# Optimization experiments

Measured on AMD Instinct MI355X. Metric: run time of the kernel, lower is better.

Reference implementation:

```python
import jax, jax.numpy as jnp
import numpy as np

IMAGE_SIZE = 320
SIGMA = 0.01      # soft-edge width in NDC units (~1.6 px at 320 res)
CHUNK = 128       # faces per scan step (bounds peak memory)


def setup_inputs() -> dict:
    key = jax.random.key(0)
    k1, k2 = jax.random.split(key)
    verts = jax.random.normal(k1, (4, 778, 3), dtype=jnp.float32) * 0.5
    faces = jax.random.randint(k2, (1538, 3), 0, 778, dtype=jnp.int32)
    return {"verts": verts, "faces": faces}


def _silhouette(verts, faces):
    B = verts.shape[0]
    S = IMAGE_SIZE
    # NMR.forward flips the y axis of verts before rendering
    v = verts * jnp.array([1.0, -1.0, 1.0], dtype=verts.dtype)
    xy = v[..., :2]  # orthographic projection (perspective=False)
    F = faces.shape[0]
    n_chunks = -(-F // CHUNK)
    Fp = n_chunks * CHUNK
    faces_p = jnp.pad(faces, ((0, Fp - F), (0, 0)))
    valid = (jnp.arange(Fp) < F).astype(verts.dtype)
    tri = xy[:, faces_p]  # [B, Fp, 3, 2]
    tri = jnp.moveaxis(tri.reshape(B, n_chunks, CHUNK, 3, 2), 1, 0)  # [nc,B,C,3,2]
    valid = valid.reshape(n_chunks, CHUNK)
    # pixel centers in NDC [-1, 1]
    lin = (jnp.arange(S, dtype=verts.dtype) + 0.5) / S * 2.0 - 1.0
    py, px = jnp.meshgrid(lin, lin, indexing="ij")
    px = px.reshape(-1)  # [P]
    py = py.reshape(-1)

    def edge_d(a, b, sgn):
        # signed distance of every pixel to oriented edge a->b: [B, C, P]
        ex = b[..., 0] - a[..., 0]
        ey = b[..., 1] - a[..., 1]
        inv_len = 1.0 / (jnp.sqrt(ex * ex + ey * ey) + 1e-8)
        d = (ex[..., None] * (py[None, None, :] - a[..., 1:2])
             - ey[..., None] * (px[None, None, :] - a[..., 0:1]))
        return sgn[..., None] * d * inv_len[..., None]

    def body(acc, chunk):
        tri_c, m = chunk  # [B,C,3,2], [C]
        v0, v1, v2 = tri_c[..., 0, :], tri_c[..., 1, :], tri_c[..., 2, :]
        # orientation sign so CW / CCW triangles are handled uniformly
        area2 = ((v1[..., 0] - v0[..., 0]) * (v2[..., 1] - v0[..., 1])
                 - (v1[..., 1] - v0[..., 1]) * (v2[..., 0] - v0[..., 0]))
        sgn = jnp.sign(area2)
        logp = (jax.nn.log_sigmoid(edge_d(v0, v1, sgn) / SIGMA)
                + jax.nn.log_sigmoid(edge_d(v1, v2, sgn) / SIGMA)
                + jax.nn.log_sigmoid(edge_d(v2, v0, sgn) / SIGMA))
        prob = jnp.clip(jnp.exp(logp) * m[None, :, None], 0.0, 1.0 - 1e-6)
        return acc + jnp.sum(jnp.log1p(-prob), axis=1), None

    acc0 = jnp.zeros((B, S * S), dtype=verts.dtype)
    acc, _ = jax.lax.scan(body, acc0, (tri, valid))
    # silhouette = 1 - prod_f (1 - coverage_f), accumulated in log space
    return (1.0 - jnp.exp(acc)).reshape(B, S, S)


def reference(verts, faces):
    return _silhouette(verts, faces)
```

## Files before the change

### kernel.cpp

```cpp
#include <hip/hip_runtime.h>
#include <math.h>


#define IMG_S 320
#define N_FACES 1538
#define N_VERTS 778
#define N_BATCH 4
#define FP 1600
#define TILE 8
#define CHUNK_F 384
#define N_CHUNKS 4
#define MAXB 388
#define NWAVE 4
#define INV_SIGMA 100.0f
#define T_CUT 12.0f
#define ACC_CUT_P 2.2603294e-6f
#define LOG2_1EM6 -19.9315686f

__global__ __launch_bounds__(256)
void prep_faces(const float* __restrict__ verts,
                const int* __restrict__ faces,
                float4* __restrict__ gE0,
                float4* __restrict__ gE1,
                float4* __restrict__ gE2)
{
    const int f = blockIdx.x * 256 + threadIdx.x;
    const int b = blockIdx.z;
    if (f >= N_FACES) return;

    const float* vb = verts + (size_t)b * N_VERTS * 3;
    const int i0 = faces[f * 3 + 0];
    const int i1 = faces[f * 3 + 1];
    const int i2 = faces[f * 3 + 2];
    const float x0 = vb[i0 * 3 + 0], y0 = -vb[i0 * 3 + 1];
    const float x1 = vb[i1 * 3 + 0], y1 = -vb[i1 * 3 + 1];
    const float x2 = vb[i2 * 3 + 0], y2 = -vb[i2 * 3 + 1];

    const float dx1 = x1 - x0, dy1 = y1 - y0;
    const float dx2 = x2 - x0, dy2 = y2 - y0;
    const float area2 = __builtin_fmaf(dx1, dy2, -__fmul_rn(dy1, dx2));
    const float sgn = (area2 > 0.0f) ? 1.0f : ((area2 < 0.0f) ? -1.0f : 0.0f);

    const size_t o = (size_t)b * FP + f;
    {
        const float ex = x1 - x0, ey = y1 - y0;
        const float s = sgn * INV_SIGMA / (sqrtf(ex * ex + ey * ey) + 1e-8f);
        gE0[o] = make_float4(-s * ey, s * ex, s * (ey * x0 - ex * y0), 0.0f);
    }
    {
        const float ex = x2 - x1, ey = y2 - y1;
        const float s = sgn * INV_SIGMA / (sqrtf(ex * ex + ey * ey) + 1e-8f);
        gE1[o] = make_float4(-s * ey, s * ex, s * (ey * x1 - ex * y1), 0.0f);
    }
    {
        const float ex = x0 - x2, ey = y0 - y2;
        const float s = sgn * INV_SIGMA / (sqrtf(ex * ex + ey * ey) + 1e-8f);
        gE2[o] = make_float4(-s * ey, s * ex, s * (ey * x2 - ex * y2), 0.0f);
    }
}

__global__ __launch_bounds__(256)
void silhouette_ws(const float4* __restrict__ gE0,
                   const float4* __restrict__ gE1,
                   const float4* __restrict__ gE2,
                   float* __restrict__ out)
{
    __shared__ float4 sE0[MAXB];
    __shared__ float4 sE1[MAXB];
    __shared__ float4 sE2[MAXB];
    __shared__ float sAcc[256];
    __shared__ int sCount;
    __shared__ int sAlive;
    __shared__ int sCover;

    const int t    = threadIdx.x;
    const int wave = t >> 6;
    const int lane = t & 63;
    const int p    = t & 63;
    const int plx  = p & 7;
    const int ply  = p >> 3;
    const int b    = blockIdx.z;
    const int gx   = blockIdx.x * TILE + plx;
    const int gy   = blockIdx.y * TILE + ply;

    const float w  = 2.0f / IMG_S;
    const float px = (gx + 0.5f) * w - 1.0f;
    const float py = (gy + 0.5f) * w - 1.0f;
    const float cx = (blockIdx.x * TILE + 4) * w - 1.0f;
    const float cy = (blockIdx.y * TILE + 4) * w - 1.0f;
    const float rr = 3.5f * w;

    const float4* gb0 = gE0 + (size_t)b * FP;
    const float4* gb1 = gE1 + (size_t)b * FP;
    const float4* gb2 = gE2 + (size_t)b * FP;

    float acc = 1.0f;

    for (int c = 0; c < N_CHUNKS; ++c) {
        const int base = c * CHUNK_F;
        const int end  = (c == N_CHUNKS - 1) ? N_FACES : base + CHUNK_F;

        sAcc[t] = acc;
        if (t == 0) { sCount = 0; sAlive = 0; sCover = 0; }
        __syncthreads();

        const float tot = sAcc[p] * sAcc[p + 64] * sAcc[p + 128] * sAcc[p + 192];
        const bool alive = (tot > ACC_CUT_P);
        if (alive) sAlive = 1;
        __syncthreads();

        if (sAlive == 0) break;

        for (int fb = base; fb < end; fb += 256) {
            const int fc = fb + t;
            const bool vald = (fc < end);
            const int fcc = vald ? fc : (end - 1);
            const float4 e0 = gb0[fcc];
            const float4 e1 = gb1[fcc];
            const float4 e2 = gb2[fcc];
            const float c0 = fmaf(e0.x, cx, fmaf(e0.y, cy, e0.z));
            const float c1 = fmaf(e1.x, cx, fmaf(e1.y, cy, e1.z));
            const float c2 = fmaf(e2.x, cx, fmaf(e2.y, cy, e2.z));
            const float r0 = rr * (fabsf(e0.x) + fabsf(e0.y));
            const float r1 = rr * (fabsf(e1.x) + fabsf(e1.y));
            const float r2 = rr * (fabsf(e2.x) + fabsf(e2.y));
            const float m_hi = fminf(c0 + r0, fminf(c1 + r1, c2 + r2));
            const float m_lo = fminf(c0 - r0, fminf(c1 - r1, c2 - r2));
            const bool isCov  = vald && (m_lo > T_CUT);
            const bool isBand = vald && !isCov && (m_hi > -T_CUT);

            const unsigned long long mb = __ballot(isBand);
            int wbase = 0;
            if (lane == 0) {
                const int nw = __popcll(mb);
                if (nw) wbase = atomicAdd(&sCount, nw);
            }
            wbase = __shfl(wbase, 0);
            if (isBand) {
                const int pos = wbase + __popcll(mb & ((1ull << lane) - 1ull));
                sE0[pos] = e0;
                sE1[pos] = e1;
                sE2[pos] = e2;
            }
            const unsigned long long mc = __ballot(isCov);
            if (lane == 0) {
                const int ncv = __popcll(mc);
                if (ncv) atomicAdd(&sCover, ncv);
            }
        }
        __syncthreads();

        const float coverF = exp2f((float)sCover * LOG2_1EM6);
        bool live = alive && (acc * coverF > ACC_CUT_P);
        if (wave == 0) acc *= coverF;

        const int n = sCount;
        int j = wave;
        while (j < n) {
            if (__ballot(live) == 0ull) break;
            const int j1 = j + NWAVE;
            const int j1c = (j1 < n) ? j1 : j;
            const float4 A0 = sE0[j],   A1 = sE1[j],   A2 = sE2[j];
            const float4 B0 = sE0[j1c], B1 = sE1[j1c], B2 = sE2[j1c];
            {
                const float xa = fmaf(A0.x, px, fmaf(A0.y, py, A0.z));
                const float xb = fmaf(A1.x, px, fmaf(A1.y, py, A1.z));
                const float xc = fmaf(A2.x, px, fmaf(A2.y, py, A2.z));
                const float m = fminf(xa, fminf(xb, xc));
                if (live && m > -T_CUT) {
                    const float da = 1.0f + __expf(-xa);
                    const float db = 1.0f + __expf(-xb);
                    const float dc = 1.0f + __expf(-xc);
                    const float f = fmaxf(
                        1.0f - __builtin_amdgcn_rcpf(da * db * dc), 1e-6f);
                    acc *= f;
                    live = (acc > ACC_CUT_P);
                }
            }
            if (j1 < n) {
                const float xa = fmaf(B0.x, px, fmaf(B0.y, py, B0.z));
                const float xb = fmaf(B1.x, px, fmaf(B1.y, py, B1.z));
                const float xc = fmaf(B2.x, px, fmaf(B2.y, py, B2.z));
                const float m = fminf(xa, fminf(xb, xc));
                if (live && m > -T_CUT) {
                    const float da = 1.0f + __expf(-xa);
                    const float db = 1.0f + __expf(-xb);
                    const float dc = 1.0f + __expf(-xc);
                    const float f = fmaxf(
                        1.0f - __builtin_amdgcn_rcpf(da * db * dc), 1e-6f);
                    acc *= f;
                    live = (acc > ACC_CUT_P);
                }
            }
            j += 2 * NWAVE;
        }
    }

    sAcc[t] = acc;
    __syncthreads();
    if (t < 64) {
        const float tot = sAcc[p] * sAcc[p + 64] * sAcc[p + 128] * sAcc[p + 192];
        out[(size_t)b * (IMG_S * IMG_S) + (size_t)gy * IMG_S + gx] = 1.0f - tot;
    }
}

extern "C" void kernel_launch(void* const* d_in, const int* in_sizes, int n_in,
                              void* d_out, int out_size, void* d_ws, size_t ws_size,
                              hipStream_t stream) {
    const float* verts = (const float*)d_in[0];
    const int* faces = (const int*)d_in[1];
    float* out = (float*)d_out;

    float4* gE0 = (float4*)d_ws;
    float4* gE1 = gE0 + (size_t)N_BATCH * FP;
    float4* gE2 = gE1 + (size_t)N_BATCH * FP;

    dim3 pgrid((N_FACES + 255) / 256, 1, N_BATCH);
    prep_faces<<<pgrid, 256, 0, stream>>>(verts, faces, gE0, gE1, gE2);

    dim3 grid(IMG_S / TILE, IMG_S / TILE, N_BATCH);
    silhouette_ws<<<grid, 256, 0, stream>>>(gE0, gE1, gE2, out);
}
```

Baseline: 81.74 us.

## Classify active edges per tile and specialize per-face sigmoid evaluation

Edge coefficients are pre-scaled by log2(e)/sigma so the inner loop uses exp2 directly. During binning, each band face records which of its edges can still affect the tile (the others are treated as saturated at 1), and the per-pixel loop branches uniformly on that count to evaluate one, two or three sigmoids. Per-pixel live tracking is replaced by a wave-wide early-exit check on the accumulator. This cuts exp, rcp and LDS reads for faces near a single edge, at the cost of extra branching and a slightly different approximation near the cutoffs.

```diff
diff --git a/kernel.cpp b/kernel.cpp
--- a/kernel.cpp
+++ b/kernel.cpp
@@ -12,8 +12,9 @@
 #define N_CHUNKS 4
 #define MAXB 388
 #define NWAVE 4
-#define INV_SIGMA 100.0f
-#define T_CUT 12.0f
+#define SCALE_S 144.2695041f
+#define T_CUT_S 17.31234049f
+#define T_ACT_S 18.75503553f
 #define ACC_CUT_P 2.2603294e-6f
 #define LOG2_1EM6 -19.9315686f
 
@@ -44,17 +45,17 @@
     const size_t o = (size_t)b * FP + f;
     {
         const float ex = x1 - x0, ey = y1 - y0;
-        const float s = sgn * INV_SIGMA / (sqrtf(ex * ex + ey * ey) + 1e-8f);
+        const float s = sgn * SCALE_S / (sqrtf(ex * ex + ey * ey) + 1e-8f);
         gE0[o] = make_float4(-s * ey, s * ex, s * (ey * x0 - ex * y0), 0.0f);
     }
     {
         const float ex = x2 - x1, ey = y2 - y1;
-        const float s = sgn * INV_SIGMA / (sqrtf(ex * ex + ey * ey) + 1e-8f);
+        const float s = sgn * SCALE_S / (sqrtf(ex * ex + ey * ey) + 1e-8f);
         gE1[o] = make_float4(-s * ey, s * ex, s * (ey * x1 - ex * y1), 0.0f);
     }
     {
         const float ex = x0 - x2, ey = y0 - y2;
-        const float s = sgn * INV_SIGMA / (sqrtf(ex * ex + ey * ey) + 1e-8f);
+        const float s = sgn * SCALE_S / (sqrtf(ex * ex + ey * ey) + 1e-8f);
         gE2[o] = make_float4(-s * ey, s * ex, s * (ey * x2 - ex * y2), 0.0f);
     }
 }
@@ -126,8 +127,8 @@
             const float r2 = rr * (fabsf(e2.x) + fabsf(e2.y));
             const float m_hi = fminf(c0 + r0, fminf(c1 + r1, c2 + r2));
             const float m_lo = fminf(c0 - r0, fminf(c1 - r1, c2 - r2));
-            const bool isCov  = vald && (m_lo > T_CUT);
-            const bool isBand = vald && !isCov && (m_hi > -T_CUT);
+            const bool isCov  = vald && (m_lo > T_CUT_S);
+            const bool isBand = vald && !isCov && (m_hi > -T_CUT_S);
 
             const unsigned long long mb = __ballot(isBand);
             int wbase = 0;
@@ -138,8 +139,15 @@
             wbase = __shfl(wbase, 0);
             if (isBand) {
                 const int pos = wbase + __popcll(mb & ((1ull << lane) - 1ull));
-                sE0[pos] = e0;
-                sE1[pos] = e1;
+                const bool a0 = (c0 - r0) <= T_ACT_S;
+                const bool a1 = (c1 - r1) <= T_ACT_S;
+                const bool a2 = (c2 - r2) <= T_ACT_S;
+                const int cnt = (int)a0 + (int)a1 + (int)a2;
+                float4 first  = a0 ? e0 : (a1 ? e1 : e2);
+                const float4 second = a0 ? (a1 ? e1 : e2) : e2;
+                first.w = __int_as_float(cnt);
+                sE0[pos] = first;
+                sE1[pos] = second;
                 sE2[pos] = e2;
             }
             const unsigned long long mc = __ballot(isCov);
@@ -151,45 +159,74 @@
         __syncthreads();
 
         const float coverF = exp2f((float)sCover * LOG2_1EM6);
-        bool live = alive && (acc * coverF > ACC_CUT_P);
         if (wave == 0) acc *= coverF;
 
         const int n = sCount;
         int j = wave;
         while (j < n) {
-            if (__ballot(live) == 0ull) break;
+            if (__ballot(acc > ACC_CUT_P) == 0ull) break;
             const int j1 = j + NWAVE;
             const int j1c = (j1 < n) ? j1 : j;
-            const float4 A0 = sE0[j],   A1 = sE1[j],   A2 = sE2[j];
-            const float4 B0 = sE0[j1c], B1 = sE1[j1c], B2 = sE2[j1c];
+            const float4 A0 = sE0[j];
+            const float4 B0 = sE0[j1c];
             {
-                const float xa = fmaf(A0.x, px, fmaf(A0.y, py, A0.z));
-                const float xb = fmaf(A1.x, px, fmaf(A1.y, py, A1.z));
-                const float xc = fmaf(A2.x, px, fmaf(A2.y, py, A2.z));
-                const float m = fminf(xa, fminf(xb, xc));
-                if (live && m > -T_CUT) {
-                    const float da = 1.0f + __expf(-xa);
-                    const float db = 1.0f + __expf(-xb);
-                    const float dc = 1.0f + __expf(-xc);
-                    const float f = fmaxf(
-                        1.0f - __builtin_amdgcn_rcpf(da * db * dc), 1e-6f);
-                    acc *= f;
-                    live = (acc > ACC_CUT_P);
+                const float x0 = fmaf(A0.x, px, fmaf(A0.y, py, A0.z));
+                const int cnt = __builtin_amdgcn_readfirstlane(
+                                    __float_as_int(A0.w));
+                if (cnt == 1) {
+                    acc *= fmaxf(__builtin_amdgcn_rcpf(1.0f + exp2f(x0)),
+                                 1e-6f);
+                } else {
+                    const float4 A1 = sE1[j];
+                    const float x1 = fmaf(A1.x, px, fmaf(A1.y, py, A1.z));
+                    if (cnt == 2) {
+                        const float d0 = 1.0f + exp2f(-x0);
+                        const float d1 = 1.0f + exp2f(-x1);
+                        acc *= fmaxf(
+                            1.0f - __builtin_amdgcn_rcpf(d0 * d1), 1e-6f);
+                    } else {
+                        const float4 A2 = sE2[j];
+                        const float x2 = fmaf(A2.x, px, fmaf(A2.y, py, A2.z));
+                        const float m = fminf(x0, fminf(x1, x2));
+                        if (m > -T_CUT_S) {
+                            const float d0 = 1.0f + exp2f(-x0);
+                            const float d1 = 1.0f + exp2f(-x1);
+                            const float d2 = 1.0f + exp2f(-x2);
+                            acc *= fmaxf(
+                                1.0f - __builtin_amdgcn_rcpf(d0 * d1 * d2),
+                                1e-6f);
+                        }
+                    }
                 }
             }
             if (j1 < n) {
-                const float xa = fmaf(B0.x, px, fmaf(B0.y, py, B0.z));
-                const float xb = fmaf(B1.x, px, fmaf(B1.y, py, B1.z));
-                const float xc = fmaf(B2.x, px, fmaf(B2.y, py, B2.z));
-                const float m = fminf(xa, fminf(xb, xc));
-                if (live && m > -T_CUT) {
-                    const float da = 1.0f + __expf(-xa);
-                    const float db = 1.0f + __expf(-xb);
-                    const float dc = 1.0f + __expf(-xc);
-                    const float f = fmaxf(
-                        1.0f - __builtin_amdgcn_rcpf(da * db * dc), 1e-6f);
-                    acc *= f;
-                    live = (acc > ACC_CUT_P);
+                const float x0 = fmaf(B0.x, px, fmaf(B0.y, py, B0.z));
+                const int cnt = __builtin_amdgcn_readfirstlane(
+                                    __float_as_int(B0.w));
+                if (cnt == 1) {
+                    acc *= fmaxf(__builtin_amdgcn_rcpf(1.0f + exp2f(x0)),
+                                 1e-6f);
+                } else {
+                    const float4 B1 = sE1[j1c];
+                    const float x1 = fmaf(B1.x, px, fmaf(B1.y, py, B1.z));
+                    if (cnt == 2) {
+                        const float d0 = 1.0f + exp2f(-x0);
+                        const float d1 = 1.0f + exp2f(-x1);
+                        acc *= fmaxf(
+                            1.0f - __builtin_amdgcn_rcpf(d0 * d1), 1e-6f);
+                    } else {
+                        const float4 B2 = sE2[j1c];
+                        const float x2 = fmaf(B2.x, px, fmaf(B2.y, py, B2.z));
+                        const float m = fminf(x0, fminf(x1, x2));
+                        if (m > -T_CUT_S) {
+                            const float d0 = 1.0f + exp2f(-x0);
+                            const float d1 = 1.0f + exp2f(-x1);
+                            const float d2 = 1.0f + exp2f(-x2);
+                            acc *= fmaxf(
+                                1.0f - __builtin_amdgcn_rcpf(d0 * d1 * d2),
+                                1e-6f);
+                        }
+                    }
                 }
             }
             j += 2 * NWAVE;
```

New measurement: 134.1 us. 64.1% more time.

## Split band faces into single-edge and multi-edge lists with base-2 edge scaling

Applied to the files above, without the earlier changes.

Edge coefficients are pre-scaled by log2(e)/sigma so the per-pixel sigmoid uses exp2 directly. During face binning, each band face is classified by how many of its edges can be active over the tile. Faces where at most one edge matters store only that edge and are evaluated with a single exp and rcp per pixel. Faces with two or more active edges go into a second list packed from the top of a shared buffer. The per-pixel live flag is replaced by a wave-level ballot on acc, which removes per-face branching but lets pixels that have already saturated keep multiplying.

```diff
diff --git a/kernel.cpp b/kernel.cpp
--- a/kernel.cpp
+++ b/kernel.cpp
@@ -12,8 +12,9 @@
 #define N_CHUNKS 4
 #define MAXB 388
 #define NWAVE 4
-#define INV_SIGMA 100.0f
-#define T_CUT 12.0f
+#define SCALE_S 144.2695041f
+#define T_CUT_S 17.31234049f
+#define T_ACT_S 18.75503553f
 #define ACC_CUT_P 2.2603294e-6f
 #define LOG2_1EM6 -19.9315686f
 
@@ -44,17 +45,17 @@
     const size_t o = (size_t)b * FP + f;
     {
         const float ex = x1 - x0, ey = y1 - y0;
-        const float s = sgn * INV_SIGMA / (sqrtf(ex * ex + ey * ey) + 1e-8f);
+        const float s = sgn * SCALE_S / (sqrtf(ex * ex + ey * ey) + 1e-8f);
         gE0[o] = make_float4(-s * ey, s * ex, s * (ey * x0 - ex * y0), 0.0f);
     }
     {
         const float ex = x2 - x1, ey = y2 - y1;
-        const float s = sgn * INV_SIGMA / (sqrtf(ex * ex + ey * ey) + 1e-8f);
+        const float s = sgn * SCALE_S / (sqrtf(ex * ex + ey * ey) + 1e-8f);
         gE1[o] = make_float4(-s * ey, s * ex, s * (ey * x1 - ex * y1), 0.0f);
     }
     {
         const float ex = x0 - x2, ey = y0 - y2;
-        const float s = sgn * INV_SIGMA / (sqrtf(ex * ex + ey * ey) + 1e-8f);
+        const float s = sgn * SCALE_S / (sqrtf(ex * ex + ey * ey) + 1e-8f);
         gE2[o] = make_float4(-s * ey, s * ex, s * (ey * x2 - ex * y2), 0.0f);
     }
 }
@@ -65,11 +66,10 @@
                    const float4* __restrict__ gE2,
                    float* __restrict__ out)
 {
-    __shared__ float4 sE0[MAXB];
-    __shared__ float4 sE1[MAXB];
-    __shared__ float4 sE2[MAXB];
+    __shared__ float4 sBuf[3 * MAXB];
     __shared__ float sAcc[256];
-    __shared__ int sCount;
+    __shared__ int sCount1;
+    __shared__ int sCount3;
     __shared__ int sAlive;
     __shared__ int sCover;
 
@@ -101,7 +101,7 @@
         const int end  = (c == N_CHUNKS - 1) ? N_FACES : base + CHUNK_F;
 
         sAcc[t] = acc;
-        if (t == 0) { sCount = 0; sAlive = 0; sCover = 0; }
+        if (t == 0) { sCount1 = 0; sCount3 = 0; sAlive = 0; sCover = 0; }
         __syncthreads();
 
         const float tot = sAcc[p] * sAcc[p + 64] * sAcc[p + 128] * sAcc[p + 192];
@@ -126,21 +126,44 @@
             const float r2 = rr * (fabsf(e2.x) + fabsf(e2.y));
             const float m_hi = fminf(c0 + r0, fminf(c1 + r1, c2 + r2));
             const float m_lo = fminf(c0 - r0, fminf(c1 - r1, c2 - r2));
-            const bool isCov  = vald && (m_lo > T_CUT);
-            const bool isBand = vald && !isCov && (m_hi > -T_CUT);
-
-            const unsigned long long mb = __ballot(isBand);
-            int wbase = 0;
-            if (lane == 0) {
-                const int nw = __popcll(mb);
-                if (nw) wbase = atomicAdd(&sCount, nw);
-            }
-            wbase = __shfl(wbase, 0);
-            if (isBand) {
-                const int pos = wbase + __popcll(mb & ((1ull << lane) - 1ull));
-                sE0[pos] = e0;
-                sE1[pos] = e1;
-                sE2[pos] = e2;
+            const bool isCov  = vald && (m_lo > T_CUT_S);
+            const bool isBand = vald && !isCov && (m_hi > -T_CUT_S);
+
+            const bool a0 = (c0 - r0) <= T_ACT_S;
+            const bool a1 = (c1 - r1) <= T_ACT_S;
+            const bool a2 = (c2 - r2) <= T_ACT_S;
+            const int cnt = (int)a0 + (int)a1 + (int)a2;
+            const bool isS = isBand && (cnt <= 1);
+            const bool isT = isBand && (cnt >= 2);
+
+            {
+                const unsigned long long ms = __ballot(isS);
+                int wb = 0;
+                if (lane == 0) {
+                    const int nw = __popcll(ms);
+                    if (nw) wb = atomicAdd(&sCount1, nw);
+                }
+                wb = __shfl(wb, 0);
+                if (isS) {
+                    const int pos = wb + __popcll(ms & ((1ull << lane) - 1ull));
+                    sBuf[pos] = a0 ? e0 : (a1 ? e1 : e2);
+                }
+            }
+            {
+                const unsigned long long mt = __ballot(isT);
+                int wb = 0;
+                if (lane == 0) {
+                    const int nw = __popcll(mt);
+                    if (nw) wb = atomicAdd(&sCount3, nw);
+                }
+                wb = __shfl(wb, 0);
+                if (isT) {
+                    const int pos = wb + __popcll(mt & ((1ull << lane) - 1ull));
+                    const int bix = 3 * MAXB - 3 * (pos + 1);
+                    sBuf[bix + 0] = e0;
+                    sBuf[bix + 1] = e1;
+                    sBuf[bix + 2] = e2;
+                }
             }
             const unsigned long long mc = __ballot(isCov);
             if (lane == 0) {
@@ -151,45 +174,61 @@
         __syncthreads();
 
         const float coverF = exp2f((float)sCover * LOG2_1EM6);
-        bool live = alive && (acc * coverF > ACC_CUT_P);
         if (wave == 0) acc *= coverF;
 
-        const int n = sCount;
+        const int n1 = sCount1;
         int j = wave;
-        while (j < n) {
-            if (__ballot(live) == 0ull) break;
+        while (j < n1) {
+            if (__ballot(acc > ACC_CUT_P) == 0ull) break;
             const int j1 = j + NWAVE;
-            const int j1c = (j1 < n) ? j1 : j;
-            const float4 A0 = sE0[j],   A1 = sE1[j],   A2 = sE2[j];
-            const float4 B0 = sE0[j1c], B1 = sE1[j1c], B2 = sE2[j1c];
+            const int j1c = (j1 < n1) ? j1 : j;
+            const float4 A = sBuf[j];
+            const float4 B = sBuf[j1c];
+            {
+                const float x = fmaf(A.x, px, fmaf(A.y, py, A.z));
+                acc *= fmaxf(__builtin_amdgcn_rcpf(1.0f + exp2f(x)), 1e-6f);
+            }
+            if (j1 < n1) {
+                const float x = fmaf(B.x, px, fmaf(B.y, py, B.z));
+                acc *= fmaxf(__builtin_amdgcn_rcpf(1.0f + exp2f(x)), 1e-6f);
+            }
+            j += 2 * NWAVE;
+        }
+
+        const int n3 = sCount3;
+        j = wave;
+        while (j < n3) {
+            if (__ballot(acc > ACC_CUT_P) == 0ull) break;
+            const int j1 = j + NWAVE;
+            const int j1c = (j1 < n3) ? j1 : j;
+            const int bx0 = 3 * MAXB - 3 * (j + 1);
+            const int bx1 = 3 * MAXB - 3 * (j1c + 1);
+            const float4 A0 = sBuf[bx0], A1 = sBuf[bx0 + 1], A2 = sBuf[bx0 + 2];
+            const float4 B0 = sBuf[bx1], B1 = sBuf[bx1 + 1], B2 = sBuf[bx1 + 2];
             {
                 const float xa = fmaf(A0.x, px, fmaf(A0.y, py, A0.z));
                 const float xb = fmaf(A1.x, px, fmaf(A1.y, py, A1.z));
                 const float xc = fmaf(A2.x, px, fmaf(A2.y, py, A2.z));
                 const float m = fminf(xa, fminf(xb, xc));
-                if (live && m > -T_CUT) {
-                    const float da = 1.0f + __expf(-xa);
-                    const float db = 1.0f + __expf(-xb);
-                    const float dc = 1.0f + __expf(-xc);
-                    const float f = fmaxf(
+                if (m > -T_CUT_S) {
+                    const float da = 1.0f + exp2f(-xa);
+                    const float db = 1.0f + exp2f(-xb);
+                    const float dc = 1.0f + exp2f(-xc);
+                    acc *= fmaxf(
                         1.0f - __builtin_amdgcn_rcpf(da * db * dc), 1e-6f);
-                    acc *= f;
-                    live = (acc > ACC_CUT_P);
-                }
-            }
-            if (j1 < n) {
+                }
+            }
+            if (j1 < n3) {
                 const float xa = fmaf(B0.x, px, fmaf(B0.y, py, B0.z));
                 const float xb = fmaf(B1.x, px, fmaf(B1.y, py, B1.z));
                 const float xc = fmaf(B2.x, px, fmaf(B2.y, py, B2.z));
                 const float m = fminf(xa, fminf(xb, xc));
-                if (live && m > -T_CUT) {
-                    const float da = 1.0f + __expf(-xa);
-                    const float db = 1.0f + __expf(-xb);
-                    const float dc = 1.0f + __expf(-xc);
-                    const float f = fmaxf(
+                if (m > -T_CUT_S) {
+                    const float da = 1.0f + exp2f(-xa);
+                    const float db = 1.0f + exp2f(-xb);
+                    const float dc = 1.0f + exp2f(-xc);
+                    acc *= fmaxf(
                         1.0f - __builtin_amdgcn_rcpf(da * db * dc), 1e-6f);
-                    acc *= f;
-                    live = (acc > ACC_CUT_P);
                 }
             }
             j += 2 * NWAVE;
```

Measured after the change: 128.8 us. 57.5% more time.
